# Kernel optimization log

Measured on AMD Instinct MI355X. Metric: run time of the kernel, lower is better.

The kernel has to match this reference:

```python
import jax, jax.numpy as jnp
import numpy as np

N_NODES = 100000
N_EDGES = 1600000
FEATURE = 32
HIDDEN = 64
CLASSES = 10
K = 3  # TAGConv default number of hops


def setup_inputs() -> dict:
    key = jax.random.key(0)
    k1, k2, k3, k4, k5, k6, k7 = jax.random.split(key, 7)
    x = jax.random.normal(k1, (N_NODES, FEATURE), dtype=jnp.float32)
    edge_index = jax.random.randint(k2, (2, N_EDGES), 0, N_NODES, dtype=jnp.int32)
    # TAGConv holds K+1 linear maps (one per hop power) plus a bias.
    s1 = 1.0 / np.sqrt(FEATURE)
    s2 = 1.0 / np.sqrt(HIDDEN)
    W1 = jax.random.uniform(k3, (K + 1, FEATURE, HIDDEN), jnp.float32, -s1, s1)
    b1 = jax.random.uniform(k4, (HIDDEN,), jnp.float32, -s1, s1)
    W2 = jax.random.uniform(k5, (K + 1, HIDDEN, CLASSES), jnp.float32, -s2, s2)
    b2 = jax.random.uniform(k6, (CLASSES,), jnp.float32, -s2, s2)
    return {"x": x, "edge_index": edge_index, "W1": W1, "b1": b1, "W2": W2, "b2": b2}


def _tagconv(x, row, col, norm, W, b):
    # out = sum_k (A_hat^k x) W_k + b, A_hat = D^-1/2 A D^-1/2 (no self loops)
    out = x @ W[0]
    h = x
    for k in range(1, W.shape[0]):
        h = jnp.zeros_like(h).at[col].add(norm[:, None] * h[row])
        out = out + h @ W[k]
    return out + b


def reference(x, edge_index, W1, b1, W2, b2):
    row, col = edge_index[0], edge_index[1]
    n = x.shape[0]
    # gcn_norm with unit edge weights, add_self_loops=False
    deg = jnp.zeros((n,), x.dtype).at[col].add(1.0)
    dinv = jnp.where(deg > 0, jax.lax.rsqrt(jnp.maximum(deg, 1.0)), 0.0)
    norm = dinv[row] * dinv[col]

    h = _tagconv(x, row, col, norm, W1, b1)
    h = jax.nn.relu(h)
    # dropout is identity in eval mode
    h = _tagconv(h, row, col, norm, W2, b2)
    return jax.nn.log_softmax(h, axis=1)
```

## Files before the change

### kernel.cpp

```cpp
#include <hip/hip_runtime.h>

typedef unsigned int uint;
typedef short s8v __attribute__((ext_vector_type(8)));
typedef float f4v __attribute__((ext_vector_type(4)));

#define N_NODES 100000
#define N_EDGES 1600000
#define FEAT 32
#define HID 64
#define NCLS 10

#define BUCKET_SHIFT 8
#define NBUCKET 391
#define NCB 256
#define CHUNK ((N_EDGES + NCB - 1) / NCB)
#define BH_N (NBUCKET * NCB)
#define NB_BH ((BH_N + 255) / 256)
#define CAP 6144
#define LROW 65


__device__ __forceinline__ uint pack_bf16(float lo, float hi) {
    uint a = __float_as_uint(lo);
    uint b = __float_as_uint(hi);
    a = a + 0x7fffu + ((a >> 16) & 1u);
    b = b + 0x7fffu + ((b >> 16) & 1u);
    return (a >> 16) | (b & 0xffff0000u);
}
__device__ __forceinline__ float unp_lo(uint v) { return __uint_as_float(v << 16); }
__device__ __forceinline__ float unp_hi(uint v) { return __uint_as_float(v & 0xffff0000u); }

__device__ __forceinline__ s8v to_s8(uint4 u) {
    union { uint4 u; s8v s; } x;
    x.u = u;
    return x.s;
}


__global__ void bucket_hist(const int* __restrict__ col, int* __restrict__ blockhist) {
    __shared__ int lh[NBUCKET];
    int blk = blockIdx.x;
    for (int i = threadIdx.x; i < NBUCKET; i += 256) lh[i] = 0;
    __syncthreads();
    int e0 = blk * CHUNK;
    int e1 = min(e0 + CHUNK, N_EDGES);
    for (int e = e0 + threadIdx.x; e < e1; e += 256)
        atomicAdd(&lh[col[e] >> BUCKET_SHIFT], 1);
    __syncthreads();
    for (int i = threadIdx.x; i < NBUCKET; i += 256)
        blockhist[i * NCB + blk] = lh[i];
}

__global__ void scanA_kernel(const int* __restrict__ src, int* __restrict__ dst,
                             int* __restrict__ bsum, int n) {
    __shared__ int s[256];
    int gid = blockIdx.x * 256 + threadIdx.x;
    int v = (gid < n) ? src[gid] : 0;
    s[threadIdx.x] = v;
    __syncthreads();
    for (int off = 1; off < 256; off <<= 1) {
        int t = (threadIdx.x >= off) ? s[threadIdx.x - off] : 0;
        __syncthreads();
        s[threadIdx.x] += t;
        __syncthreads();
    }
    if (gid < n) dst[gid] = s[threadIdx.x] - v;
    if (threadIdx.x == 255) bsum[blockIdx.x] = s[255];
}

__global__ void scanB_kernel(int* __restrict__ bsum, int nb) {
    __shared__ int s[512];
    int v = (threadIdx.x < nb) ? bsum[threadIdx.x] : 0;
    s[threadIdx.x] = v;
    __syncthreads();
    for (int off = 1; off < 512; off <<= 1) {
        int t = (threadIdx.x >= off) ? s[threadIdx.x - off] : 0;
        __syncthreads();
        s[threadIdx.x] += t;
        __syncthreads();
    }
    if (threadIdx.x < nb) bsum[threadIdx.x] = s[threadIdx.x] - v;
}

__global__ void scanC_add(int* __restrict__ dst, const int* __restrict__ bsum, int n) {
    int gid = blockIdx.x * 256 + threadIdx.x;
    if (gid < n) dst[gid] += bsum[blockIdx.x];
}

__global__ void bucket_scatter(const int* __restrict__ row, const int* __restrict__ col,
                               const int* __restrict__ base, int* __restrict__ packed) {
    __shared__ int lcnt[NBUCKET];
    __shared__ int lbase[NBUCKET];
    int blk = blockIdx.x;
    for (int i = threadIdx.x; i < NBUCKET; i += 256) {
        lcnt[i] = 0;
        lbase[i] = base[i * NCB + blk];
    }
    __syncthreads();
    int e0 = blk * CHUNK;
    int e1 = min(e0 + CHUNK, N_EDGES);
    for (int e = e0 + threadIdx.x; e < e1; e += 256) {
        int c = col[e];
        int r = row[e];
        int b = c >> BUCKET_SHIFT;
        int pos = lbase[b] + atomicAdd(&lcnt[b], 1);
        packed[pos] = (r << BUCKET_SHIFT) | (c & 255);
    }
}

__global__ void bucket_sort(const int* __restrict__ base, const int* __restrict__ packed,
                            int* __restrict__ rowptr, int* __restrict__ eidx,
                            float* __restrict__ dinv) {
    __shared__ int stage[CAP];
    __shared__ int cnt[256];
    __shared__ int lscan[256];
    int b = blockIdx.x;
    int tid = threadIdx.x;
    int s = base[b * NCB];
    int e = (b == NBUCKET - 1) ? N_EDGES : base[(b + 1) * NCB];
    int m = e - s;
    bool fits = (m <= CAP);
    cnt[tid] = 0;
    __syncthreads();
    for (int i = tid; i < m; i += 256) {
        int p = packed[s + i];
        if (fits) stage[i] = p;
        atomicAdd(&cnt[p & 255], 1);
    }
    __syncthreads();
    int node = (b << BUCKET_SHIFT) + tid;
    int c = cnt[tid];
    if (node < N_NODES) dinv[node] = (c > 0) ? rsqrtf((float)c) : 0.0f;
    lscan[tid] = c;
    __syncthreads();
    for (int off = 1; off < 256; off <<= 1) {
        int t = (tid >= off) ? lscan[tid - off] : 0;
        __syncthreads();
        lscan[tid] += t;
        __syncthreads();
    }
    int excl = lscan[tid] - c;
    if (node < N_NODES) rowptr[node] = s + excl;
    if (b == NBUCKET - 1 && tid == 0) rowptr[N_NODES] = N_EDGES;
    __syncthreads();
    lscan[tid] = excl;
    cnt[tid] = 0;
    __syncthreads();
    for (int i = tid; i < m; i += 256) {
        int p = fits ? stage[i] : packed[s + i];
        int cl = p & 255;
        int pos = lscan[cl] + atomicAdd(&cnt[cl], 1);
        eidx[s + pos] = p >> BUCKET_SHIFT;
    }
}


__global__ void prescale_kernel(const float* __restrict__ x, const float* __restrict__ dinv,
                                uint* __restrict__ t0) {
    int i = blockIdx.x * 256 + threadIdx.x;
    if (i < N_NODES * 16) {
        int node = i >> 4, fp = i & 15;
        float dv = dinv[node];
        t0[i] = pack_bf16(x[node * 32 + 2 * fp] * dv, x[node * 32 + 2 * fp + 1] * dv);
    }
}


template <int WP>
__global__ void gather32_kernel(const int* __restrict__ rowptr, const int* __restrict__ eidx,
                                const float* __restrict__ dinv, const uint* __restrict__ src,
                                uint* __restrict__ pout, uint* __restrict__ preout) {
    int node = (blockIdx.x * blockDim.x + threadIdx.x) >> 6;
    if (node >= N_NODES) return;
    int lane = threadIdx.x & 63;
    int fp = lane & 15;
    int g = lane >> 4;
    int s = rowptr[node], e = rowptr[node + 1];
    float acc0 = 0.0f, acc1 = 0.0f;
    int base = (s & ~3) + g * 4;
    for (int b = base; b < e; b += 16) {
        int4 q = *(const int4*)(eidx + b);
        uint v0 = (b     >= s && b     < e) ? src[q.x * 16 + fp] : 0u;
        uint v1 = (b + 1 >= s && b + 1 < e) ? src[q.y * 16 + fp] : 0u;
        uint v2 = (b + 2 >= s && b + 2 < e) ? src[q.z * 16 + fp] : 0u;
        uint v3 = (b + 3 >= s && b + 3 < e) ? src[q.w * 16 + fp] : 0u;
        acc0 += unp_lo(v0) + unp_lo(v1) + unp_lo(v2) + unp_lo(v3);
        acc1 += unp_hi(v0) + unp_hi(v1) + unp_hi(v2) + unp_hi(v3);
    }
    acc0 += __shfl_xor(acc0, 16);
    acc0 += __shfl_xor(acc0, 32);
    acc1 += __shfl_xor(acc1, 16);
    acc1 += __shfl_xor(acc1, 32);
    if (lane < 16) {
        float dv = dinv[node];
        pout[node * 16 + fp] = pack_bf16(dv * acc0, dv * acc1);
        if (WP) {
            float d2 = dv * dv;
            preout[node * 16 + fp] = pack_bf16(d2 * acc0, d2 * acc1);
        }
    }
}

template <int FINAL>
__global__ void gather16_kernel(const int* __restrict__ rowptr, const int* __restrict__ eidx,
                                const float* __restrict__ dinv, const uint* __restrict__ src,
                                const uint* __restrict__ add, void* __restrict__ outv) {
    int wid = (blockIdx.x * blockDim.x + threadIdx.x) >> 6;
    int lane = threadIdx.x & 63;
    int node = wid * 2 + (lane >> 5);
    if (node >= N_NODES) return;
    int fp = lane & 7;
    int g = (lane >> 3) & 3;
    int s = rowptr[node], e = rowptr[node + 1];
    float acc0 = 0.0f, acc1 = 0.0f;
    int base = (s & ~3) + g * 4;
    for (int b = base; b < e; b += 16) {
        int4 q = *(const int4*)(eidx + b);
        uint v0 = (b     >= s && b     < e) ? src[q.x * 8 + fp] : 0u;
        uint v1 = (b + 1 >= s && b + 1 < e) ? src[q.y * 8 + fp] : 0u;
        uint v2 = (b + 2 >= s && b + 2 < e) ? src[q.z * 8 + fp] : 0u;
        uint v3 = (b + 3 >= s && b + 3 < e) ? src[q.w * 8 + fp] : 0u;
        acc0 += unp_lo(v0) + unp_lo(v1) + unp_lo(v2) + unp_lo(v3);
        acc1 += unp_hi(v0) + unp_hi(v1) + unp_hi(v2) + unp_hi(v3);
    }
    acc0 += __shfl_xor(acc0, 8);
    acc0 += __shfl_xor(acc0, 16);
    acc1 += __shfl_xor(acc1, 8);
    acc1 += __shfl_xor(acc1, 16);
    float dv = dinv[node];
    uint av = add[node * 8 + fp];
    float v0 = unp_lo(av) + dv * acc0;
    float v1 = unp_hi(av) + dv * acc1;
    if (!FINAL) {
        if (g == 0) ((uint*)outv)[node * 8 + fp] = pack_bf16(dv * v0, dv * v1);
    } else {
        float l0 = (2 * fp     < NCLS) ? v0 : -1e30f;
        float l1 = (2 * fp + 1 < NCLS) ? v1 : -1e30f;
        float m = fmaxf(l0, l1);
        m = fmaxf(m, __shfl_xor(m, 1));
        m = fmaxf(m, __shfl_xor(m, 2));
        m = fmaxf(m, __shfl_xor(m, 4));
        float ex = ((2 * fp     < NCLS) ? __expf(l0 - m) : 0.0f)
                 + ((2 * fp + 1 < NCLS) ? __expf(l1 - m) : 0.0f);
        ex += __shfl_xor(ex, 1);
        ex += __shfl_xor(ex, 2);
        ex += __shfl_xor(ex, 4);
        float ls = logf(ex) + m;
        if (g == 0 && fp < 5) {
            float2 o = {l0 - ls, l1 - ls};
            *(float2*)((float*)outv + (size_t)node * 10 + 2 * fp) = o;
        }
    }
}


__global__ void wfprep_kernel(const float* __restrict__ W1, const float* __restrict__ W2,
                              uint* __restrict__ wf1, uint* __restrict__ wf2) {
    int idx = blockIdx.x * 256 + threadIdx.x;
    if (idx < 4096) {
        int vj = idx & 3, frag = idx >> 2;
        int lane = frag & 63, ks = (frag >> 6) & 3, nt = frag >> 8;
        int g = lane >> 4, c = lane & 15;
        int k0 = ks * 32 + g * 8 + 2 * vj;
        int n = nt * 16 + c;
        wf1[idx] = pack_bf16(W1[k0 * 64 + n], W1[(k0 + 1) * 64 + n]);
    } else if (idx < 6144) {
        int i2 = idx - 4096;
        int vj = i2 & 3, frag = i2 >> 2;
        int lane = frag & 63, ks = (frag >> 6) & 1, nt = frag >> 7;
        int g = lane >> 4, c = lane & 15;
        int k0 = ks * 32 + g * 8 + 2 * vj;
        float v0 = (c < NCLS) ? W2[(nt * HID + k0) * NCLS + c] : 0.0f;
        float v1 = (c < NCLS) ? W2[(nt * HID + k0 + 1) * NCLS + c] : 0.0f;
        wf2[i2] = pack_bf16(v0, v1);
    }
}


__global__ __launch_bounds__(256) void dense_fused(
        const float* __restrict__ x, const uint* __restrict__ p1,
        const uint* __restrict__ p2, const uint* __restrict__ p3,
        const uint* __restrict__ wf1, const uint* __restrict__ wf2,
        const float* __restrict__ b1, const float* __restrict__ b2,
        const float* __restrict__ dinv, uint* __restrict__ z, int zstride) {
    __shared__ float hls[4 * 16 * LROW];
    int tid = threadIdx.x;
    int wv = tid >> 6, l = tid & 63, g = l >> 4, c = l & 15;
    float* my = hls + wv * 16 * LROW;
    int row0 = blockIdx.x * 64 + wv * 16;
    int ra = row0 + c;
    int rc = min(ra, N_NODES - 1);

    uint4 au0;
    {
        float4 xa = *(const float4*)(x + rc * 32 + g * 8);
        float4 xb = *(const float4*)(x + rc * 32 + g * 8 + 4);
        au0.x = pack_bf16(xa.x, xa.y);
        au0.y = pack_bf16(xa.z, xa.w);
        au0.z = pack_bf16(xb.x, xb.y);
        au0.w = pack_bf16(xb.z, xb.w);
    }
    uint4 au1 = *(const uint4*)(p1 + rc * 16 + g * 4);
    uint4 au2 = *(const uint4*)(p2 + rc * 16 + g * 4);
    uint4 au3 = *(const uint4*)(p3 + rc * 16 + g * 4);
    s8v a0 = to_s8(au0), a1 = to_s8(au1), a2 = to_s8(au2), a3 = to_s8(au3);

    f4v acc[4];
#pragma unroll
    for (int nt = 0; nt < 4; nt++) {
        f4v ac = {0.f, 0.f, 0.f, 0.f};
        const s8v* wp = (const s8v*)(wf1 + (nt * 4) * 64 * 4 + l * 4);
        ac = __builtin_amdgcn_mfma_f32_16x16x32_bf16(a0, wp[0 * 64], ac, 0, 0, 0);
        ac = __builtin_amdgcn_mfma_f32_16x16x32_bf16(a1, wp[1 * 64], ac, 0, 0, 0);
        ac = __builtin_amdgcn_mfma_f32_16x16x32_bf16(a2, wp[2 * 64], ac, 0, 0, 0);
        ac = __builtin_amdgcn_mfma_f32_16x16x32_bf16(a3, wp[3 * 64], ac, 0, 0, 0);
        acc[nt] = ac;
    }

#pragma unroll
    for (int nt = 0; nt < 4; nt++) {
        float bb = b1[nt * 16 + c];
#pragma unroll
        for (int reg = 0; reg < 4; reg++) {
            my[(4 * g + reg) * LROW + nt * 16 + c] = fmaxf(acc[nt][reg] + bb, 0.0f);
        }
    }
    __syncthreads();

    uint4 b2u[2];
#pragma unroll
    for (int ks = 0; ks < 2; ks++) {
        float4 h0 = *(const float4*)&my[c * LROW + ks * 32 + g * 8];
        float4 h1 = *(const float4*)&my[c * LROW + ks * 32 + g * 8 + 4];
        b2u[ks].x = pack_bf16(h0.x, h0.y);
        b2u[ks].y = pack_bf16(h0.z, h0.w);
        b2u[ks].z = pack_bf16(h1.x, h1.y);
        b2u[ks].w = pack_bf16(h1.z, h1.w);
    }
    s8v h0f = to_s8(b2u[0]), h1f = to_s8(b2u[1]);

    f4v acc2[4];
#pragma unroll
    for (int nt = 0; nt < 4; nt++) {
        f4v ac = {0.f, 0.f, 0.f, 0.f};
        const s8v* wp = (const s8v*)(wf2 + (nt * 2) * 64 * 4 + l * 4);
        ac = __builtin_amdgcn_mfma_f32_16x16x32_bf16(h0f, wp[0 * 64], ac, 0, 0, 0);
        ac = __builtin_amdgcn_mfma_f32_16x16x32_bf16(h1f, wp[1 * 64], ac, 0, 0, 0);
        acc2[nt] = ac;
    }

#pragma unroll
    for (int nt = 0; nt < 4; nt++) {
        float bb = (nt == 0 && c < NCLS) ? b2[c] : 0.0f;
        uint* zk = z + (size_t)nt * zstride;
#pragma unroll
        for (int reg = 0; reg < 4; reg++) {
            int rr = row0 + 4 * g + reg;
            float v = acc2[nt][reg] + bb;
            if (nt == 3) v *= dinv[min(rr, N_NODES - 1)];
            float vn = __shfl_xor(v, 1);
            if (rr < N_NODES && (c & 1) == 0) {
                zk[rr * 8 + (c >> 1)] = pack_bf16(v, vn);
            }
        }
    }
}


extern "C" void kernel_launch(void* const* d_in, const int* in_sizes, int n_in,
                              void* d_out, int out_size, void* d_ws, size_t ws_size,
                              hipStream_t stream) {
    const float* x  = (const float*)d_in[0];
    const int*   ei = (const int*)d_in[1];
    const float* W1 = (const float*)d_in[2];
    const float* b1 = (const float*)d_in[3];
    const float* W2 = (const float*)d_in[4];
    const float* b2 = (const float*)d_in[5];
    float* out = (float*)d_out;

    const int* row = ei;
    const int* col = ei + N_EDGES;

    float* w = (float*)d_ws;
    size_t o = 0;
    auto alloc = [&](size_t nel) { float* p = w + o; o += (nel + 63) & ~(size_t)63; return p; };

    int*   rowptr = (int*)alloc(N_NODES + 1);
    int*   bsum   = (int*)alloc(512);
    float* dinv   = alloc(N_NODES);
    uint*  wf1    = (uint*)alloc(4096);
    uint*  wf2    = (uint*)alloc(2048);
    int*   eidx   = (int*)alloc(N_EDGES + 16);
    float* bufA   = alloc((size_t)N_NODES * 32);
    float* bufB   = alloc((size_t)N_NODES * 32);
    float* bufC   = alloc((size_t)N_NODES * 32);
    float* bufD   = alloc((size_t)N_NODES * 32);
    float* h      = alloc((size_t)N_NODES * HID);

    int* blockhist = (int*)bufB;
    int* bhbase    = (int*)bufC;
    int* packed    = (int*)h;

    uint* t0  = (uint*)bufA;
    uint* p1  = (uint*)bufB;
    uint* p1p = (uint*)bufC;
    uint* p2  = (uint*)bufD;
    uint* p2p = (uint*)bufA;
    uint* p3  = (uint*)bufC;
    const int ZS = N_NODES * 8;
    uint* z0  = (uint*)h;
    uint* z1  = (uint*)h + ZS;
    uint* z2  = (uint*)h + 2 * (size_t)ZS;
    uint* z3p = (uint*)h + 3 * (size_t)ZS;
    uint* tAp = (uint*)bufC;
    uint* tBp = (uint*)bufC + ZS;

    const int TB = 256;
    const int gW = (N_NODES * 64) / TB;
    const int gW2 = ((N_NODES + 1) / 2 * 64 + TB - 1) / TB;

    bucket_hist<<<NCB, TB, 0, stream>>>(col, blockhist);
    scanA_kernel<<<NB_BH, TB, 0, stream>>>(blockhist, bhbase, bsum, BH_N);
    scanB_kernel<<<1, 512, 0, stream>>>(bsum, NB_BH);
    scanC_add<<<NB_BH, TB, 0, stream>>>(bhbase, bsum, BH_N);
    bucket_scatter<<<NCB, TB, 0, stream>>>(row, col, bhbase, packed);
    bucket_sort<<<NBUCKET, TB, 0, stream>>>(bhbase, packed, rowptr, eidx, dinv);

    wfprep_kernel<<<24, TB, 0, stream>>>(W1, W2, wf1, wf2);

    prescale_kernel<<<(N_NODES * 16 + TB - 1) / TB, TB, 0, stream>>>(x, dinv, t0);
    gather32_kernel<1><<<gW, TB, 0, stream>>>(rowptr, eidx, dinv, t0,  p1, p1p);
    gather32_kernel<1><<<gW, TB, 0, stream>>>(rowptr, eidx, dinv, p1p, p2, p2p);
    gather32_kernel<0><<<gW, TB, 0, stream>>>(rowptr, eidx, dinv, p2p, p3, nullptr);

    int gF = (N_NODES + 63) / 64;
    dense_fused<<<gF, TB, 0, stream>>>(x, p1, p2, p3, wf1, wf2, b1, b2, dinv, z0, ZS);

    gather16_kernel<0><<<gW2, TB, 0, stream>>>(rowptr, eidx, dinv, z3p, z2, tAp);
    gather16_kernel<0><<<gW2, TB, 0, stream>>>(rowptr, eidx, dinv, tAp, z1, tBp);
    gather16_kernel<1><<<gW2, TB, 0, stream>>>(rowptr, eidx, dinv, tBp, z0, out);
}
```

Before: 285.1 us.

## Compress CSR edge indices to 16-bit with per-node high-bit split and persistent gathers

The bucket sort now orders each node's incoming edges by whether the source index is at least 65536. It stores only the low 16 bits of each source plus a per-node count of low-half edges, and the gather kernels rebuild the full index from the edge position. This halves the index bytes read in all six gather passes. The gathers also become grid-stride loops with a fixed block count instead of one wave per node. The cost is some extra compare logic per edge, a second 16-bit array to read, and a sort that now uses 512 keys.

```diff
diff --git a/kernel.cpp b/kernel.cpp
--- a/kernel.cpp
+++ b/kernel.cpp
@@ -1,6 +1,7 @@
 #include <hip/hip_runtime.h>
 
 typedef unsigned int uint;
+typedef unsigned short ushort_t;
 typedef short s8v __attribute__((ext_vector_type(8)));
 typedef float f4v __attribute__((ext_vector_type(4)));
 
@@ -19,6 +20,9 @@
 #define CAP 6144
 #define LROW 65
 
+#define G32_BLOCKS 6144
+#define G16_BLOCKS 3072
+
 
 __device__ __forceinline__ uint pack_bf16(float lo, float hi) {
     uint a = __float_as_uint(lo);
@@ -109,48 +113,58 @@
 }
 
 __global__ void bucket_sort(const int* __restrict__ base, const int* __restrict__ packed,
-                            int* __restrict__ rowptr, int* __restrict__ eidx,
-                            float* __restrict__ dinv) {
+                            int* __restrict__ rowptr, ushort_t* __restrict__ elo,
+                            ushort_t* __restrict__ nmid, float* __restrict__ dinv) {
     __shared__ int stage[CAP];
-    __shared__ int cnt[256];
-    __shared__ int lscan[256];
+    __shared__ int cnt[512];
+    __shared__ int excl[512];
+    __shared__ int psum[256];
     int b = blockIdx.x;
     int tid = threadIdx.x;
     int s = base[b * NCB];
     int e = (b == NBUCKET - 1) ? N_EDGES : base[(b + 1) * NCB];
     int m = e - s;
-    bool fits = (m <= CAP);
     cnt[tid] = 0;
+    cnt[tid + 256] = 0;
     __syncthreads();
     for (int i = tid; i < m; i += 256) {
         int p = packed[s + i];
-        if (fits) stage[i] = p;
-        atomicAdd(&cnt[p & 255], 1);
-    }
-    __syncthreads();
+        if (i < CAP) stage[i] = p;
+        int r = p >> BUCKET_SHIFT;
+        int key = ((p & 255) << 1) | (r >= 65536);
+        atomicAdd(&cnt[key], 1);
+    }
+    __syncthreads();
+    int c0 = cnt[2 * tid], c1 = cnt[2 * tid + 1];
+    psum[tid] = c0 + c1;
+    __syncthreads();
+    for (int off = 1; off < 256; off <<= 1) {
+        int t = (tid >= off) ? psum[tid - off] : 0;
+        __syncthreads();
+        psum[tid] += t;
+        __syncthreads();
+    }
+    int tot = c0 + c1;
+    int pex = psum[tid] - tot;
+    excl[2 * tid] = pex;
+    excl[2 * tid + 1] = pex + c0;
     int node = (b << BUCKET_SHIFT) + tid;
-    int c = cnt[tid];
-    if (node < N_NODES) dinv[node] = (c > 0) ? rsqrtf((float)c) : 0.0f;
-    lscan[tid] = c;
-    __syncthreads();
-    for (int off = 1; off < 256; off <<= 1) {
-        int t = (tid >= off) ? lscan[tid - off] : 0;
-        __syncthreads();
-        lscan[tid] += t;
-        __syncthreads();
-    }
-    int excl = lscan[tid] - c;
-    if (node < N_NODES) rowptr[node] = s + excl;
+    if (node < N_NODES) {
+        dinv[node] = (tot > 0) ? rsqrtf((float)tot) : 0.0f;
+        rowptr[node] = s + pex;
+        nmid[node] = (ushort_t)c0;
+    }
     if (b == NBUCKET - 1 && tid == 0) rowptr[N_NODES] = N_EDGES;
     __syncthreads();
-    lscan[tid] = excl;
     cnt[tid] = 0;
+    cnt[tid + 256] = 0;
     __syncthreads();
     for (int i = tid; i < m; i += 256) {
-        int p = fits ? stage[i] : packed[s + i];
-        int cl = p & 255;
-        int pos = lscan[cl] + atomicAdd(&cnt[cl], 1);
-        eidx[s + pos] = p >> BUCKET_SHIFT;
+        int p = (i < CAP) ? stage[i] : packed[s + i];
+        int r = p >> BUCKET_SHIFT;
+        int key = ((p & 255) << 1) | (r >= 65536);
+        int pos = excl[key] + atomicAdd(&cnt[key], 1);
+        elo[s + pos] = (ushort_t)r;
     }
 }
 
@@ -167,88 +181,106 @@
 
 
 template <int WP>
-__global__ void gather32_kernel(const int* __restrict__ rowptr, const int* __restrict__ eidx,
+__global__ void gather32_kernel(const int* __restrict__ rowptr, const ushort_t* __restrict__ elo,
+                                const ushort_t* __restrict__ nmid,
                                 const float* __restrict__ dinv, const uint* __restrict__ src,
                                 uint* __restrict__ pout, uint* __restrict__ preout) {
-    int node = (blockIdx.x * blockDim.x + threadIdx.x) >> 6;
-    if (node >= N_NODES) return;
+    int wid = (blockIdx.x * 256 + threadIdx.x) >> 6;
     int lane = threadIdx.x & 63;
     int fp = lane & 15;
     int g = lane >> 4;
-    int s = rowptr[node], e = rowptr[node + 1];
-    float acc0 = 0.0f, acc1 = 0.0f;
-    int base = (s & ~3) + g * 4;
-    for (int b = base; b < e; b += 16) {
-        int4 q = *(const int4*)(eidx + b);
-        uint v0 = (b     >= s && b     < e) ? src[q.x * 16 + fp] : 0u;
-        uint v1 = (b + 1 >= s && b + 1 < e) ? src[q.y * 16 + fp] : 0u;
-        uint v2 = (b + 2 >= s && b + 2 < e) ? src[q.z * 16 + fp] : 0u;
-        uint v3 = (b + 3 >= s && b + 3 < e) ? src[q.w * 16 + fp] : 0u;
-        acc0 += unp_lo(v0) + unp_lo(v1) + unp_lo(v2) + unp_lo(v3);
-        acc1 += unp_hi(v0) + unp_hi(v1) + unp_hi(v2) + unp_hi(v3);
-    }
-    acc0 += __shfl_xor(acc0, 16);
-    acc0 += __shfl_xor(acc0, 32);
-    acc1 += __shfl_xor(acc1, 16);
-    acc1 += __shfl_xor(acc1, 32);
-    if (lane < 16) {
-        float dv = dinv[node];
-        pout[node * 16 + fp] = pack_bf16(dv * acc0, dv * acc1);
-        if (WP) {
-            float d2 = dv * dv;
-            preout[node * 16 + fp] = pack_bf16(d2 * acc0, d2 * acc1);
+    const int NW = G32_BLOCKS * 4;
+    for (int node = wid; node < N_NODES; node += NW) {
+        int s = rowptr[node], e = rowptr[node + 1];
+        int smid = s + nmid[node];
+        float acc0 = 0.0f, acc1 = 0.0f;
+        int base = (s & ~3) + g * 4;
+        for (int b = base; b < e; b += 16) {
+            ushort4 q = *(const ushort4*)(elo + b);
+            int i0 = q.x | ((b     >= smid) ? 0x10000 : 0);
+            int i1 = q.y | ((b + 1 >= smid) ? 0x10000 : 0);
+            int i2 = q.z | ((b + 2 >= smid) ? 0x10000 : 0);
+            int i3 = q.w | ((b + 3 >= smid) ? 0x10000 : 0);
+            uint v0 = (b     >= s && b     < e) ? src[i0 * 16 + fp] : 0u;
+            uint v1 = (b + 1 >= s && b + 1 < e) ? src[i1 * 16 + fp] : 0u;
+            uint v2 = (b + 2 >= s && b + 2 < e) ? src[i2 * 16 + fp] : 0u;
+            uint v3 = (b + 3 >= s && b + 3 < e) ? src[i3 * 16 + fp] : 0u;
+            acc0 += unp_lo(v0) + unp_lo(v1) + unp_lo(v2) + unp_lo(v3);
+            acc1 += unp_hi(v0) + unp_hi(v1) + unp_hi(v2) + unp_hi(v3);
+        }
+        acc0 += __shfl_xor(acc0, 16);
+        acc0 += __shfl_xor(acc0, 32);
+        acc1 += __shfl_xor(acc1, 16);
+        acc1 += __shfl_xor(acc1, 32);
+        if (lane < 16) {
+            float dv = dinv[node];
+            pout[node * 16 + fp] = pack_bf16(dv * acc0, dv * acc1);
+            if (WP) {
+                float d2 = dv * dv;
+                preout[node * 16 + fp] = pack_bf16(d2 * acc0, d2 * acc1);
+            }
         }
     }
 }
 
 template <int FINAL>
-__global__ void gather16_kernel(const int* __restrict__ rowptr, const int* __restrict__ eidx,
+__global__ void gather16_kernel(const int* __restrict__ rowptr, const ushort_t* __restrict__ elo,
+                                const ushort_t* __restrict__ nmid,
                                 const float* __restrict__ dinv, const uint* __restrict__ src,
                                 const uint* __restrict__ add, void* __restrict__ outv) {
-    int wid = (blockIdx.x * blockDim.x + threadIdx.x) >> 6;
+    int wid = (blockIdx.x * 256 + threadIdx.x) >> 6;
     int lane = threadIdx.x & 63;
-    int node = wid * 2 + (lane >> 5);
-    if (node >= N_NODES) return;
     int fp = lane & 7;
     int g = (lane >> 3) & 3;
-    int s = rowptr[node], e = rowptr[node + 1];
-    float acc0 = 0.0f, acc1 = 0.0f;
-    int base = (s & ~3) + g * 4;
-    for (int b = base; b < e; b += 16) {
-        int4 q = *(const int4*)(eidx + b);
-        uint v0 = (b     >= s && b     < e) ? src[q.x * 8 + fp] : 0u;
-        uint v1 = (b + 1 >= s && b + 1 < e) ? src[q.y * 8 + fp] : 0u;
-        uint v2 = (b + 2 >= s && b + 2 < e) ? src[q.z * 8 + fp] : 0u;
-        uint v3 = (b + 3 >= s && b + 3 < e) ? src[q.w * 8 + fp] : 0u;
-        acc0 += unp_lo(v0) + unp_lo(v1) + unp_lo(v2) + unp_lo(v3);
-        acc1 += unp_hi(v0) + unp_hi(v1) + unp_hi(v2) + unp_hi(v3);
-    }
-    acc0 += __shfl_xor(acc0, 8);
-    acc0 += __shfl_xor(acc0, 16);
-    acc1 += __shfl_xor(acc1, 8);
-    acc1 += __shfl_xor(acc1, 16);
-    float dv = dinv[node];
-    uint av = add[node * 8 + fp];
-    float v0 = unp_lo(av) + dv * acc0;
-    float v1 = unp_hi(av) + dv * acc1;
-    if (!FINAL) {
-        if (g == 0) ((uint*)outv)[node * 8 + fp] = pack_bf16(dv * v0, dv * v1);
-    } else {
-        float l0 = (2 * fp     < NCLS) ? v0 : -1e30f;
-        float l1 = (2 * fp + 1 < NCLS) ? v1 : -1e30f;
-        float m = fmaxf(l0, l1);
-        m = fmaxf(m, __shfl_xor(m, 1));
-        m = fmaxf(m, __shfl_xor(m, 2));
-        m = fmaxf(m, __shfl_xor(m, 4));
-        float ex = ((2 * fp     < NCLS) ? __expf(l0 - m) : 0.0f)
-                 + ((2 * fp + 1 < NCLS) ? __expf(l1 - m) : 0.0f);
-        ex += __shfl_xor(ex, 1);
-        ex += __shfl_xor(ex, 2);
-        ex += __shfl_xor(ex, 4);
-        float ls = logf(ex) + m;
-        if (g == 0 && fp < 5) {
-            float2 o = {l0 - ls, l1 - ls};
-            *(float2*)((float*)outv + (size_t)node * 10 + 2 * fp) = o;
+    int half = lane >> 5;
+    const int NW = G16_BLOCKS * 4;
+    const int NPAIR = N_NODES / 2;
+    for (int p = wid; p < NPAIR; p += NW) {
+        int node = p * 2 + half;
+        int s = rowptr[node], e = rowptr[node + 1];
+        int smid = s + nmid[node];
+        float acc0 = 0.0f, acc1 = 0.0f;
+        int base = (s & ~3) + g * 4;
+        for (int b = base; b < e; b += 16) {
+            ushort4 q = *(const ushort4*)(elo + b);
+            int i0 = q.x | ((b     >= smid) ? 0x10000 : 0);
+            int i1 = q.y | ((b + 1 >= smid) ? 0x10000 : 0);
+            int i2 = q.z | ((b + 2 >= smid) ? 0x10000 : 0);
+            int i3 = q.w | ((b + 3 >= smid) ? 0x10000 : 0);
+            uint v0 = (b     >= s && b     < e) ? src[i0 * 8 + fp] : 0u;
+            uint v1 = (b + 1 >= s && b + 1 < e) ? src[i1 * 8 + fp] : 0u;
+            uint v2 = (b + 2 >= s && b + 2 < e) ? src[i2 * 8 + fp] : 0u;
+            uint v3 = (b + 3 >= s && b + 3 < e) ? src[i3 * 8 + fp] : 0u;
+            acc0 += unp_lo(v0) + unp_lo(v1) + unp_lo(v2) + unp_lo(v3);
+            acc1 += unp_hi(v0) + unp_hi(v1) + unp_hi(v2) + unp_hi(v3);
+        }
+        acc0 += __shfl_xor(acc0, 8);
+        acc0 += __shfl_xor(acc0, 16);
+        acc1 += __shfl_xor(acc1, 8);
+        acc1 += __shfl_xor(acc1, 16);
+        float dv = dinv[node];
+        uint av = add[node * 8 + fp];
+        float v0 = unp_lo(av) + dv * acc0;
+        float v1 = unp_hi(av) + dv * acc1;
+        if (!FINAL) {
+            if (g == 0) ((uint*)outv)[node * 8 + fp] = pack_bf16(dv * v0, dv * v1);
+        } else {
+            float l0 = (2 * fp     < NCLS) ? v0 : -1e30f;
+            float l1 = (2 * fp + 1 < NCLS) ? v1 : -1e30f;
+            float m = fmaxf(l0, l1);
+            m = fmaxf(m, __shfl_xor(m, 1));
+            m = fmaxf(m, __shfl_xor(m, 2));
+            m = fmaxf(m, __shfl_xor(m, 4));
+            float ex = ((2 * fp     < NCLS) ? __expf(l0 - m) : 0.0f)
+                     + ((2 * fp + 1 < NCLS) ? __expf(l1 - m) : 0.0f);
+            ex += __shfl_xor(ex, 1);
+            ex += __shfl_xor(ex, 2);
+            ex += __shfl_xor(ex, 4);
+            float ls = logf(ex) + m;
+            if (g == 0 && fp < 5) {
+                float2 o = {l0 - ls, l1 - ls};
+                *(float2*)((float*)outv + (size_t)node * 10 + 2 * fp) = o;
+            }
         }
     }
 }
@@ -385,17 +417,18 @@
     size_t o = 0;
     auto alloc = [&](size_t nel) { float* p = w + o; o += (nel + 63) & ~(size_t)63; return p; };
 
-    int*   rowptr = (int*)alloc(N_NODES + 1);
-    int*   bsum   = (int*)alloc(512);
-    float* dinv   = alloc(N_NODES);
-    uint*  wf1    = (uint*)alloc(4096);
-    uint*  wf2    = (uint*)alloc(2048);
-    int*   eidx   = (int*)alloc(N_EDGES + 16);
-    float* bufA   = alloc((size_t)N_NODES * 32);
-    float* bufB   = alloc((size_t)N_NODES * 32);
-    float* bufC   = alloc((size_t)N_NODES * 32);
-    float* bufD   = alloc((size_t)N_NODES * 32);
-    float* h      = alloc((size_t)N_NODES * HID);
+    int*      rowptr = (int*)alloc(N_NODES + 1);
+    int*      bsum   = (int*)alloc(512);
+    float*    dinv   = alloc(N_NODES);
+    ushort_t* nmid   = (ushort_t*)alloc(50048);
+    uint*     wf1    = (uint*)alloc(4096);
+    uint*     wf2    = (uint*)alloc(2048);
+    ushort_t* elo    = (ushort_t*)alloc(800064);
+    float*    bufA   = alloc((size_t)N_NODES * 32);
+    float*    bufB   = alloc((size_t)N_NODES * 32);
+    float*    bufC   = alloc((size_t)N_NODES * 32);
+    float*    bufD   = alloc((size_t)N_NODES * 32);
+    float*    h      = alloc((size_t)N_NODES * HID);
 
     int* blockhist = (int*)bufB;
     int* bhbase    = (int*)bufC;
@@ -416,27 +449,25 @@
     uint* tBp = (uint*)bufC + ZS;
 
     const int TB = 256;
-    const int gW = (N_NODES * 64) / TB;
-    const int gW2 = ((N_NODES + 1) / 2 * 64 + TB - 1) / TB;
 
     bucket_hist<<<NCB, TB, 0, stream>>>(col, blockhist);
     scanA_kernel<<<NB_BH, TB, 0, stream>>>(blockhist, bhbase, bsum, BH_N);
     scanB_kernel<<<1, 512, 0, stream>>>(bsum, NB_BH);
     scanC_add<<<NB_BH, TB, 0, stream>>>(bhbase, bsum, BH_N);
     bucket_scatter<<<NCB, TB, 0, stream>>>(row, col, bhbase, packed);
-    bucket_sort<<<NBUCKET, TB, 0, stream>>>(bhbase, packed, rowptr, eidx, dinv);
+    bucket_sort<<<NBUCKET, TB, 0, stream>>>(bhbase, packed, rowptr, elo, nmid, dinv);
 
     wfprep_kernel<<<24, TB, 0, stream>>>(W1, W2, wf1, wf2);
 
     prescale_kernel<<<(N_NODES * 16 + TB - 1) / TB, TB, 0, stream>>>(x, dinv, t0);
-    gather32_kernel<1><<<gW, TB, 0, stream>>>(rowptr, eidx, dinv, t0,  p1, p1p);
-    gather32_kernel<1><<<gW, TB, 0, stream>>>(rowptr, eidx, dinv, p1p, p2, p2p);
-    gather32_kernel<0><<<gW, TB, 0, stream>>>(rowptr, eidx, dinv, p2p, p3, nullptr);
+    gather32_kernel<1><<<G32_BLOCKS, TB, 0, stream>>>(rowptr, elo, nmid, dinv, t0,  p1, p1p);
+    gather32_kernel<1><<<G32_BLOCKS, TB, 0, stream>>>(rowptr, elo, nmid, dinv, p1p, p2, p2p);
+    gather32_kernel<0><<<G32_BLOCKS, TB, 0, stream>>>(rowptr, elo, nmid, dinv, p2p, p3, nullptr);
 
     int gF = (N_NODES + 63) / 64;
     dense_fused<<<gF, TB, 0, stream>>>(x, p1, p2, p3, wf1, wf2, b1, b2, dinv, z0, ZS);
 
-    gather16_kernel<0><<<gW2, TB, 0, stream>>>(rowptr, eidx, dinv, z3p, z2, tAp);
-    gather16_kernel<0><<<gW2, TB, 0, stream>>>(rowptr, eidx, dinv, tAp, z1, tBp);
-    gather16_kernel<1><<<gW2, TB, 0, stream>>>(rowptr, eidx, dinv, tBp, z0, out);
-}
+    gather16_kernel<0><<<G16_BLOCKS, TB, 0, stream>>>(rowptr, elo, nmid, dinv, z3p, z2, tAp);
+    gather16_kernel<0><<<G16_BLOCKS, TB, 0, stream>>>(rowptr, elo, nmid, dinv, tAp, z1, tBp);
+    gather16_kernel<1><<<G16_BLOCKS, TB, 0, stream>>>(rowptr, elo, nmid, dinv, tBp, z0, out);
+}
```

After: 291.0 us. +2.1%, slower.
